# Optimization experiments

Measured on AMD Instinct MI355X. Metric: run time of the kernel, lower is better.

## Reference

```python
import jax, jax.numpy as jnp
import numpy as np

EPS = 1e-5


def setup_inputs() -> dict:
    key = jax.random.key(0)
    ks = jax.random.split(key, 12)
    B, S, M, D, H, dh = 8, 512, 512, 1024, 16, 64
    T = S + M
    w_scale = 0.03  # keep attention logits in a sane range (mimics nn.Linear init scale)
    return {
        "x": jax.random.normal(ks[0], (B, S, D), jnp.float32),
        "mem": jax.random.normal(ks[1], (B, M, D), jnp.float32),
        "R": jax.random.normal(ks[2], (T, D), jnp.float32),
        "u": jax.random.normal(ks[3], (1, H, 1, dh), jnp.float32) * 0.1,
        "t": jax.random.normal(ks[4], (1, H, 1, dh), jnp.float32) * 0.1,
        "Wq": jax.random.normal(ks[5], (H * dh, D), jnp.float32) * w_scale,
        "Wk": jax.random.normal(ks[6], (H * dh, D), jnp.float32) * w_scale,
        "Wv": jax.random.normal(ks[7], (H * dh, D), jnp.float32) * w_scale,
        "Wr": jax.random.normal(ks[8], (H * dh, D), jnp.float32) * w_scale,
        "Wo": jax.random.normal(ks[9], (D, H * dh), jnp.float32) * w_scale,
        "gamma": jnp.ones((D,), jnp.float32),
        "beta": jnp.zeros((D,), jnp.float32),
    }


def reference(x, mem, R, u, t, Wq, Wk, Wv, Wr, Wo, gamma, beta):
    B, S, D = x.shape
    H, dh = u.shape[1], u.shape[3]
    h = jnp.concatenate([mem, x], axis=1)          # [B, T, D]
    T = h.shape[1]
    M = T - S

    q = (x @ Wq.T).reshape(B, S, H, dh).transpose(0, 2, 1, 3)   # [B,H,S,dh]
    k = (h @ Wk.T).reshape(B, T, H, dh).transpose(0, 2, 1, 3)   # [B,H,T,dh]
    v = (h @ Wv.T).reshape(B, T, H, dh).transpose(0, 2, 1, 3)   # [B,H,T,dh]
    r = (R[-T:] @ Wr.T).reshape(1, T, H, dh).transpose(0, 2, 1, 3)  # [1,H,T,dh]

    ac = jnp.einsum("bhid,bhjd->bhij", q + u, k)                # [B,H,S,T]
    bd = jnp.einsum("bhid,hjd->bhij", q + t, r[0])              # [B,H,S,T]

    # circulant shift: shifted[..., i, j] = bd[..., i, (j - i + S - 1) % T]
    idx = (jnp.arange(T)[None, :] - jnp.arange(S)[:, None] + S - 1) % T  # [S,T]
    bd = jnp.take_along_axis(bd, idx[None, None], axis=3)

    # causal mask with memory offset: keep j <= i + M (tril(mem_len)), then
    # exact-zero entries (the masked ones) become -inf, matching the original.
    mask = jnp.arange(T)[None, :] <= (jnp.arange(S)[:, None] + M)        # [S,T]
    score = jnp.where(mask[None, None], (ac + bd) / jnp.sqrt(jnp.float32(dh)), 0.0)
    score = jnp.where(score == 0, -jnp.inf, score)
    p = jax.nn.softmax(score, axis=-1)                                   # [B,H,S,T]

    att = jnp.einsum("bhij,bhjd->bhid", p, v).transpose(0, 2, 1, 3).reshape(B, S, H * dh)
    out = att @ Wo.T                                                      # dropout is identity (p=0/eval)

    y = out + x
    mu = jnp.mean(y, axis=-1, keepdims=True)
    var = jnp.var(y, axis=-1, keepdims=True)
    return (y - mu) / jnp.sqrt(var + EPS) * gamma + beta
```

## Files before the change

### kernel.cpp

```cpp
#include <hip/hip_runtime.h>
#include <math.h>

#define BB 8
#define SS 512
#define MM 512
#define TT 1024
#define DD 1024
#define HH 16
#define DH 64

typedef __attribute__((ext_vector_type(8))) short bf16x8;
typedef __attribute__((ext_vector_type(4))) float f32x4;

#define SCL2E 0.1803368801111f
#define DTHR 11.5f

__device__ __forceinline__ ushort f2bf(float f) {
  union { float f; unsigned u; } x; x.f = f;
  unsigned r = x.u + 0x7fffu + ((x.u >> 16) & 1u);
  return (ushort)(r >> 16);
}
__device__ __forceinline__ float bf2f(ushort u) {
  return __builtin_bit_cast(float, ((unsigned)u) << 16);
}

__device__ __forceinline__ void stage16(void* lds, const void* g) {
  __builtin_amdgcn_global_load_lds((const __attribute__((address_space(1))) void*)g,
                                   (__attribute__((address_space(3))) void*)lds, 16, 0, 0);
}

template <int C>
__device__ __forceinline__ float dppf(float x) {
  return __builtin_bit_cast(float,
      __builtin_amdgcn_update_dpp(0, __builtin_bit_cast(int, x), C, 0xF, 0xF, true));
}
__device__ __forceinline__ float redmax16(float x) {
  x = fmaxf(x, dppf<0xB1>(x));
  x = fmaxf(x, dppf<0x4E>(x));
  x = fmaxf(x, dppf<0x141>(x));
  x = fmaxf(x, dppf<0x140>(x));
  return x;
}
__device__ __forceinline__ float redsum16(float x) {
  x += dppf<0xB1>(x);
  x += dppf<0x4E>(x);
  x += dppf<0x141>(x);
  x += dppf<0x140>(x);
  return x;
}
__device__ __forceinline__ float bperm_f(int byteaddr, float v) {
  return __builtin_bit_cast(float,
      __builtin_amdgcn_ds_bpermute(byteaddr, __builtin_bit_cast(int, v)));
}

__global__ __launch_bounds__(256) void cast_all(
    const float* __restrict__ mem, const float* __restrict__ x,
    const float* __restrict__ R, const float* __restrict__ Wq,
    const float* __restrict__ Wk, const float* __restrict__ Wv,
    const float* __restrict__ Wr, const float* __restrict__ Wo,
    ushort* __restrict__ hb, ushort* __restrict__ Rb, ushort* __restrict__ Wqb,
    ushort* __restrict__ Wkb, ushort* __restrict__ Wvb, ushort* __restrict__ Wrb,
    ushort* __restrict__ Wob) {
  const int M1 = 1 << 20;
  int i = (blockIdx.x * 256 + threadIdx.x) * 8;
  const float* src;
  ushort* dst;
  if (i < 4 * M1) {
    src = mem + i;
    dst = hb + (size_t)i + (size_t)(i >> 19) * 524288;
  } else if (i < 8 * M1) {
    int j = i - 4 * M1;
    src = x + j;
    dst = hb + (size_t)j + (size_t)(j >> 19) * 524288 + 524288;
  } else if (i < 9 * M1) {
    src = R + (i - 8 * M1);  dst = Rb + (i - 8 * M1);
  } else if (i < 10 * M1) {
    src = Wq + (i - 9 * M1); dst = Wqb + (i - 9 * M1);
  } else if (i < 11 * M1) {
    src = Wk + (i - 10 * M1); dst = Wkb + (i - 10 * M1);
  } else if (i < 12 * M1) {
    src = Wv + (i - 11 * M1); dst = Wvb + (i - 11 * M1);
  } else if (i < 13 * M1) {
    src = Wr + (i - 12 * M1); dst = Wrb + (i - 12 * M1);
  } else {
    src = Wo + (i - 13 * M1); dst = Wob + (i - 13 * M1);
  }
  float4 a = *(const float4*)(src);
  float4 c = *(const float4*)(src + 4);
  union { bf16x8 v; ushort u[8]; } pk;
  pk.u[0] = f2bf(a.x); pk.u[1] = f2bf(a.y); pk.u[2] = f2bf(a.z); pk.u[3] = f2bf(a.w);
  pk.u[4] = f2bf(c.x); pk.u[5] = f2bf(c.y); pk.u[6] = f2bf(c.z); pk.u[7] = f2bf(c.w);
  *(bf16x8*)(void*)dst = pk.v;
}

__global__ __launch_bounds__(256, 4) void gemm_qkvr(
    const ushort* __restrict__ hb, const ushort* __restrict__ Rbuf,
    const ushort* __restrict__ Wqb, const ushort* __restrict__ Wkb,
    const ushort* __restrict__ Wvb, const ushort* __restrict__ Wrb,
    ushort* __restrict__ qub,
    ushort* __restrict__ kbo, ushort* __restrict__ vtb, ushort* __restrict__ rbo,
    const float* __restrict__ uvec) {
  __shared__ ushort As0[4096], Bs0[4096], As1[4096], Bs1[4096];
  const int bid = (blockIdx.x & 7) * 168 + (blockIdx.x >> 3);
  const ushort* A;
  const ushort* W;
  ushort* C0 = nullptr;
  bool qadd = false, qslice = false, vmode = false;
  int mt, nx;
  if (bid < 256) {
    mt = bid >> 3; nx = bid & 7;
    A = hb; W = Wqb; C0 = qub; qadd = true; qslice = true;
  } else if (bid < 768) {
    int r = bid - 256; mt = r >> 3; nx = r & 7;
    A = hb; W = Wkb; C0 = kbo;
  } else if (bid < 1280) {
    int r = bid - 768; mt = r >> 3; nx = r & 7;
    A = hb; W = Wvb; C0 = vtb; vmode = true;
  } else {
    int r = bid - 1280; mt = r >> 3; nx = r & 7;
    A = Rbuf; W = Wrb; C0 = rbo;
  }
  const int m0 = mt * 128, n0 = nx * 128;

  const int t = threadIdx.x;
  const int w = t >> 6, l = t & 63;
  const int m16 = l & 15, kg = l >> 4;
  const int wr = w >> 1, wc = w & 1;

  const int c0 = t, c1 = t + 256;
  const int scol = (((t & 3) ^ ((t >> 3) & 3)) * 8);
  const ushort* asrc0;
  const ushort* asrc1;
  {
    int gm0 = m0 + (c0 >> 2), gm1 = m0 + (c1 >> 2);
    if (qslice) {
      asrc0 = A + ((size_t)((gm0 >> 9) * TT + MM + (gm0 & 511))) * DD + scol;
      asrc1 = A + ((size_t)((gm1 >> 9) * TT + MM + (gm1 & 511))) * DD + scol;
    } else {
      asrc0 = A + (size_t)gm0 * DD + scol;
      asrc1 = A + (size_t)gm1 * DD + scol;
    }
  }
  const ushort* bsrc0 = W + (size_t)(n0 + (c0 >> 2)) * DD + scol;
  const ushort* bsrc1 = W + (size_t)(n0 + (c1 >> 2)) * DD + scol;

  const int cbx = ((kg ^ ((m16 >> 1) & 3)) << 3);
  const int arow0 = (wr * 64 + m16) * 32 + cbx;
  const int brow0 = (wc * 64 + m16) * 32 + cbx;

  f32x4 acc[4][4];
#pragma unroll
  for (int mi = 0; mi < 4; ++mi)
#pragma unroll
    for (int ni = 0; ni < 4; ++ni) acc[mi][ni] = (f32x4){0.f, 0.f, 0.f, 0.f};

#define QKVR_STAGE(AS, BS, KOFF)                \
  do {                                          \
    stage16(AS + c0 * 8, asrc0 + (KOFF));       \
    stage16(AS + c1 * 8, asrc1 + (KOFF));       \
    stage16(BS + c0 * 8, bsrc0 + (KOFF));       \
    stage16(BS + c1 * 8, bsrc1 + (KOFF));       \
  } while (0)

#define QKVR_COMPUTE(AS, BS)                                                      \
  do {                                                                            \
    bf16x8 af[4], bfr[4];                                                         \
    _Pragma("unroll") for (int mi = 0; mi < 4; ++mi)                              \
        af[mi] = *(const bf16x8*)(const void*)&AS[arow0 + mi * 512];              \
    _Pragma("unroll") for (int ni = 0; ni < 4; ++ni)                              \
        bfr[ni] = *(const bf16x8*)(const void*)&BS[brow0 + ni * 512];             \
    _Pragma("unroll") for (int mi = 0; mi < 4; ++mi)                              \
        _Pragma("unroll") for (int ni = 0; ni < 4; ++ni)                          \
            acc[mi][ni] = __builtin_amdgcn_mfma_f32_16x16x32_bf16(                \
                af[mi], bfr[ni], acc[mi][ni], 0, 0, 0);                           \
  } while (0)

  QKVR_STAGE(As0, Bs0, 0);

#pragma unroll 1
  for (int kt = 0; kt < 32; kt += 2) {
    QKVR_STAGE(As1, Bs1, (kt + 1) << 5);
    asm volatile("s_waitcnt vmcnt(4)" ::: "memory");
    __builtin_amdgcn_s_barrier();
    QKVR_COMPUTE(As0, Bs0);
    __builtin_amdgcn_s_barrier();
    if (kt + 2 < 32) {
      QKVR_STAGE(As0, Bs0, (kt + 2) << 5);
      asm volatile("s_waitcnt vmcnt(4)" ::: "memory");
    } else {
      asm volatile("s_waitcnt vmcnt(0)" ::: "memory");
    }
    __builtin_amdgcn_s_barrier();
    QKVR_COMPUTE(As1, Bs1);
    __builtin_amdgcn_s_barrier();
  }
#undef QKVR_STAGE
#undef QKVR_COMPUTE

  const int rbase = m0 + wr * 64 + kg * 4;
  const int cbase = n0 + wc * 64 + m16;
  if (vmode) {
    const int bb = m0 >> 10;
    const int tt0 = (m0 & 1023) + wr * 64 + kg * 4;
#pragma unroll
    for (int mi = 0; mi < 4; ++mi)
#pragma unroll
      for (int ni = 0; ni < 4; ++ni) {
        ushort4 o;
        o.x = f2bf(acc[mi][ni][0]); o.y = f2bf(acc[mi][ni][1]);
        o.z = f2bf(acc[mi][ni][2]); o.w = f2bf(acc[mi][ni][3]);
        *(ushort4*)(C0 + ((size_t)(bb * 1024 + cbase + ni * 16) << 10) + tt0 + mi * 16) = o;
      }
  } else if (qadd) {
    float uv[4];
#pragma unroll
    for (int ni = 0; ni < 4; ++ni) uv[ni] = uvec[cbase + ni * 16];
#pragma unroll
    for (int mi = 0; mi < 4; ++mi)
#pragma unroll
      for (int ni = 0; ni < 4; ++ni)
#pragma unroll
        for (int rg = 0; rg < 4; ++rg)
          C0[(size_t)(rbase + mi * 16 + rg) * DD + cbase + ni * 16] = f2bf(acc[mi][ni][rg] + uv[ni]);
  } else {
#pragma unroll
    for (int mi = 0; mi < 4; ++mi)
#pragma unroll
      for (int ni = 0; ni < 4; ++ni)
#pragma unroll
        for (int rg = 0; rg < 4; ++rg)
          C0[(size_t)(rbase + mi * 16 + rg) * DD + cbase + ni * 16] = f2bf(acc[mi][ni][rg]);
  }
}

__global__ __launch_bounds__(256) void gemm_wo(const ushort* __restrict__ A,
                                               const ushort* __restrict__ W,
                                               ushort* __restrict__ Cb) {
  __shared__ ushort As[128 * 32];
  __shared__ ushort Bs[64 * 32];
  const int bid = (blockIdx.x & 7) * 64 + (blockIdx.x >> 3);
  const int mt = bid >> 4, nxt = bid & 15;
  const int m0 = mt * 128, n0 = nxt * 64;
  const int t = threadIdx.x;
  const int w = t >> 6, l = t & 63;
  const int m16 = l & 15, kg = l >> 4;
  const int wr = w >> 1, wc = w & 1;

  const int scol = (((t & 3) ^ ((t >> 3) & 3)) * 8);
  const ushort* asrc0 = A + (size_t)(m0 + (t >> 2)) * DD + scol;
  const ushort* asrc1 = A + (size_t)(m0 + 64 + (t >> 2)) * DD + scol;
  const ushort* bsrc0 = W + (size_t)(n0 + (t >> 2)) * DD + scol;
  ushort* adst0 = As + t * 8;
  ushort* adst1 = As + (t + 256) * 8;
  ushort* bdst0 = Bs + t * 8;

  const int cbx = ((kg ^ ((m16 >> 1) & 3)) << 3);

  f32x4 acc[4][2];
#pragma unroll
  for (int mi = 0; mi < 4; ++mi)
#pragma unroll
    for (int ni = 0; ni < 2; ++ni) acc[mi][ni] = (f32x4){0.f, 0.f, 0.f, 0.f};

  for (int k0 = 0; k0 < DD; k0 += 32) {
    stage16(adst0, asrc0 + k0);
    stage16(adst1, asrc1 + k0);
    stage16(bdst0, bsrc0 + k0);
    __syncthreads();
    bf16x8 af[4], bfr[2];
#pragma unroll
    for (int mi = 0; mi < 4; ++mi)
      af[mi] = *(const bf16x8*)(const void*)&As[(wr * 64 + mi * 16 + m16) * 32 + cbx];
#pragma unroll
    for (int ni = 0; ni < 2; ++ni)
      bfr[ni] = *(const bf16x8*)(const void*)&Bs[(wc * 32 + ni * 16 + m16) * 32 + cbx];
#pragma unroll
    for (int mi = 0; mi < 4; ++mi)
#pragma unroll
      for (int ni = 0; ni < 2; ++ni)
        acc[mi][ni] = __builtin_amdgcn_mfma_f32_16x16x32_bf16(af[mi], bfr[ni], acc[mi][ni], 0, 0, 0);
    __syncthreads();
  }

  const int rbase = m0 + wr * 64 + kg * 4;
  const int cbase = n0 + wc * 32 + m16;
#pragma unroll
  for (int mi = 0; mi < 4; ++mi)
#pragma unroll
    for (int ni = 0; ni < 2; ++ni)
#pragma unroll
      for (int rg = 0; rg < 4; ++rg)
        Cb[(size_t)(rbase + mi * 16 + rg) * DD + cbase + ni * 16] = f2bf(acc[mi][ni][rg]);
}

__global__ __launch_bounds__(256) void attn_mfma(const ushort* __restrict__ qu,
                                                 const ushort* __restrict__ kb,
                                                 const ushort* __restrict__ vt,
                                                 const ushort* __restrict__ rb,
                                                 const float* __restrict__ uvec,
                                                 const float* __restrict__ tvec,
                                                 ushort* __restrict__ att) {
  const int w = threadIdx.x >> 6;
  const int l = threadIdx.x & 63;
  const int m16 = l & 15;
  const int kg = l >> 4;
  const int bid = blockIdx.x;
  const int it = 7 - (bid >> 7);
  const int bh = bid & 127;
  const int b = bh >> 4, h = bh & 15;
  const int i0 = it * 64;

  __shared__ ushort Ks0[4096], Ks1[4096];
  __shared__ ushort Vs0[4096], Vs1[4096];
  __shared__ ushort Rl[16384];
  __shared__ ushort plds[4][16][72];

  bf16x8 aqu[2], aqt[2];
  {
    const ushort* qrow = qu + ((size_t)(b * SS + i0 + w * 16 + m16)) * DD + h * DH + kg * 8;
    aqu[0] = *(const bf16x8*)(const void*)(qrow);
    aqu[1] = *(const bf16x8*)(const void*)(qrow + 32);
#pragma unroll
    for (int ks = 0; ks < 2; ++ks) {
      ushort* a = (ushort*)&aqt[ks];
      const ushort* qa = (const ushort*)&aqu[ks];
#pragma unroll
      for (int e = 0; e < 8; ++e) {
        const int col = h * DH + kg * 8 + ks * 32 + e;
        a[e] = f2bf(bf2f(qa[e]) + (tvec[col] - uvec[col]));
      }
    }
  }

  int baddr[4];
  bool bsel[4];
#pragma unroll
  for (int rg = 0; rg < 4; ++rg) {
    const int rw = kg * 4 + rg;
    baddr[rg] = (kg * 16 + ((m16 + 15 - rw) & 15)) << 2;
    bsel[rg] = m16 > rw;
  }

  const int c0 = threadIdx.x, c1 = threadIdx.x + 256;
  const int r0 = c0 >> 3, sc0 = ((c0 & 7) * 8) ^ ((r0 & 7) << 3);
  const int r1 = c1 >> 3, sc1 = ((c1 & 7) * 8) ^ ((r1 & 7) << 3);
  const ushort* kp0 = kb + ((size_t)(b * TT) + r0) * DD + h * DH + sc0;
  const ushort* kp1 = kb + ((size_t)(b * TT) + r1) * DD + h * DH + sc1;
  const ushort* vp0 = vt + ((size_t)(b * 1024 + h * DH + r0)) * 1024 + sc0;
  const ushort* vp1 = vt + ((size_t)(b * 1024 + h * DH + r1)) * 1024 + sc1;

  const int cb0 = (kg * 8) ^ ((m16 & 7) << 3);
  const int cb1 = (kg * 8 + 32) ^ ((m16 & 7) << 3);
  int slot64[5];
#pragma unroll
  for (int f = 0; f < 5; ++f)
    slot64[f] = ((496 - i0 - w * 16 + m16 + f * 16) & 255) << 6;

  {
    const int base0 = 448 - i0;
#pragma unroll
    for (int kk = 0; kk < 4; ++kk) {
      int c = threadIdx.x + kk * 256;
      int ro = c >> 3, cc = c & 7;
      int p = base0 + ro;
      int slot = p & 255;
      stage16(Rl + slot * 64 + cc * 8,
              rb + (size_t)p * DD + h * DH + ((cc * 8) ^ ((ro & 7) << 3)));
    }
  }
  stage16(Ks0 + c0 * 8, kp0);
  stage16(Ks0 + c1 * 8, kp1);
  stage16(Vs0 + c0 * 8, vp0);
  stage16(Vs0 + c1 * 8, vp1);
  kp0 += (size_t)64 * DD; kp1 += (size_t)64 * DD;
  vp0 += 64; vp1 += 64;

  f32x4 O[4];
  float mrow[4], lrow[4];
#pragma unroll
  for (int nt = 0; nt < 4; ++nt) O[nt] = (f32x4){0.f, 0.f, 0.f, 0.f};
#pragma unroll
  for (int rg = 0; rg < 4; ++rg) { mrow[rg] = -1e30f; lrow[rg] = 0.f; }

  const int ntj = it + 9;

  auto stage_next = [&](ushort* KN, ushort* VN, int jt) {
    stage16(KN + c0 * 8, kp0);
    stage16(KN + c1 * 8, kp1);
    kp0 += (size_t)64 * DD; kp1 += (size_t)64 * DD;
    stage16(VN + c0 * 8, vp0);
    stage16(VN + c1 * 8, vp1);
    vp0 += 64; vp1 += 64;
    const int pstart = 576 + jt * 64 - i0;
#pragma unroll
    for (int kk = 0; kk < 2; ++kk) {
      int c = threadIdx.x + kk * 256;
      int ro = c >> 3, cc = c & 7;
      int p = pstart + ro;
      int pc = p < 1023 ? p : 1023;
      int slot = p & 255;
      stage16(Rl + slot * 64 + cc * 8,
              rb + (size_t)pc * DD + h * DH + ((cc * 8) ^ ((ro & 7) << 3)));
    }
  };

  auto compute_tile = [&](const ushort* kbase, const ushort* vbase, int jt) {
    const int j0 = jt * 64;
    f32x4 ac[4];
    __builtin_amdgcn_s_setprio(1);
#pragma unroll
    for (int nt = 0; nt < 4; ++nt) {
      ac[nt] = (f32x4){0.f, 0.f, 0.f, 0.f};
      const int row = nt * 16 + m16;
#pragma unroll
      for (int ks = 0; ks < 2; ++ks) {
        bf16x8 bk = *(const bf16x8*)(const void*)(kbase + row * 64 + (ks == 0 ? cb0 : cb1));
        ac[nt] = __builtin_amdgcn_mfma_f32_16x16x32_bf16(aqu[ks], bk, ac[nt], 0, 0, 0);
      }
    }
    f32x4 bd[5];
#pragma unroll
    for (int f = 0; f < 5; ++f) {
      f32x4 z = (f32x4){0.f, 0.f, 0.f, 0.f};
      bf16x8 b0 = *(const bf16x8*)(const void*)(Rl + slot64[f] + cb0);
      z = __builtin_amdgcn_mfma_f32_16x16x32_bf16(aqt[0], b0, z, 0, 0, 0);
      bf16x8 b1 = *(const bf16x8*)(const void*)(Rl + slot64[f] + cb1);
      bd[f] = __builtin_amdgcn_mfma_f32_16x16x32_bf16(aqt[1], b1, z, 0, 0, 0);
    }
    __builtin_amdgcn_s_setprio(0);
#pragma unroll
    for (int f = 0; f < 5; ++f) slot64[f] = (slot64[f] + 4096) & 16383;

    float sca[4][4];
#pragma unroll
    for (int rg = 0; rg < 4; ++rg) {
      float rr[5];
#pragma unroll
      for (int f = 0; f < 5; ++f) rr[f] = bperm_f(baddr[rg], bd[f][rg]);
#pragma unroll
      for (int nt = 0; nt < 4; ++nt) {
        float bdv = bsel[rg] ? rr[nt + 1] : rr[nt];
        sca[nt][rg] = (ac[nt][rg] + bdv) * SCL2E;
      }
    }
    if (jt == ntj - 1) {
#pragma unroll
      for (int rg = 0; rg < 4; ++rg) {
        const int jmax = i0 + w * 16 + kg * 4 + rg + MM;
#pragma unroll
        for (int nt = 0; nt < 4; ++nt)
          sca[nt][rg] = (j0 + nt * 16 + m16 <= jmax) ? sca[nt][rg] : -1e30f;
      }
    }

    float pmax[4];
#pragma unroll
    for (int rg = 0; rg < 4; ++rg) {
      float pm = fmaxf(fmaxf(sca[0][rg], sca[1][rg]), fmaxf(sca[2][rg], sca[3][rg]));
      pmax[rg] = redmax16(pm);
    }
    bool grow = false;
#pragma unroll
    for (int rg = 0; rg < 4; ++rg) grow = grow || (pmax[rg] > mrow[rg] + DTHR);
    if (__any(grow)) {
#pragma unroll
      for (int rg = 0; rg < 4; ++rg) {
        float mnew = fmaxf(mrow[rg], pmax[rg]);
        float scale = __builtin_amdgcn_exp2f(mrow[rg] - mnew);
        mrow[rg] = mnew;
        lrow[rg] *= scale;
#pragma unroll
        for (int nt = 0; nt < 4; ++nt) O[nt][rg] *= scale;
      }
    }

#pragma unroll
    for (int rg = 0; rg < 4; ++rg) {
      float ps = 0.f;
#pragma unroll
      for (int nt = 0; nt < 4; ++nt) {
        float p = __builtin_amdgcn_exp2f(sca[nt][rg] - mrow[rg]);
        ps += p;
        plds[w][kg * 4 + rg][nt * 16 + m16] = f2bf(p);
      }
      lrow[rg] += redsum16(ps);
    }

    __builtin_amdgcn_s_setprio(1);
#pragma unroll
    for (int ks = 0; ks < 2; ++ks) {
      bf16x8 pa = *(const bf16x8*)(const void*)&plds[w][m16][kg * 8 + ks * 32];
#pragma unroll
      for (int nt = 0; nt < 4; ++nt) {
        bf16x8 vf = *(const bf16x8*)(const void*)(vbase + (nt * 16 + m16) * 64 + (ks == 0 ? cb0 : cb1));
        O[nt] = __builtin_amdgcn_mfma_f32_16x16x32_bf16(pa, vf, O[nt], 0, 0, 0);
      }
    }
    __builtin_amdgcn_s_setprio(0);
  };

  int jt = 0;
  for (;;) {
    {
      if (jt + 1 < ntj) {
        stage_next(Ks1, Vs1, jt);
        asm volatile("s_waitcnt vmcnt(6)" ::: "memory");
      } else {
        asm volatile("s_waitcnt vmcnt(0)" ::: "memory");
      }
      __builtin_amdgcn_s_barrier();
      compute_tile(Ks0, Vs0, jt);
      if (jt + 1 == ntj) break;
      __builtin_amdgcn_s_barrier();
      ++jt;
    }
    {
      if (jt + 1 < ntj) {
        stage_next(Ks0, Vs0, jt);
        asm volatile("s_waitcnt vmcnt(6)" ::: "memory");
      } else {
        asm volatile("s_waitcnt vmcnt(0)" ::: "memory");
      }
      __builtin_amdgcn_s_barrier();
      compute_tile(Ks1, Vs1, jt);
      if (jt + 1 == ntj) break;
      __builtin_amdgcn_s_barrier();
      ++jt;
    }
  }

  float linv[4];
#pragma unroll
  for (int rg = 0; rg < 4; ++rg) linv[rg] = 1.f / lrow[rg];
#pragma unroll
  for (int nt = 0; nt < 4; ++nt) {
#pragma unroll
    for (int rg = 0; rg < 4; ++rg) {
      att[((size_t)(b * SS + i0 + w * 16 + kg * 4 + rg)) * DD + h * DH + nt * 16 + m16] =
          f2bf(O[nt][rg] * linv[rg]);
    }
  }
}

__global__ __launch_bounds__(256) void ln_kernel(const ushort* __restrict__ ypre,
                                                 const ushort* __restrict__ hb,
                                                 const float* __restrict__ gamma,
                                                 const float* __restrict__ beta,
                                                 float* __restrict__ out) {
  const int row = blockIdx.x;
  const int t = threadIdx.x;
  const int lane = t & 63, w = t >> 6;
  const ushort* yr = ypre + (size_t)row * DD;
  const ushort* xr = hb + ((size_t)((row >> 9) * TT + MM + (row & 511))) * DD;

  ushort4 yv = *(const ushort4*)(yr + t * 4);
  ushort4 xv = *(const ushort4*)(xr + t * 4);
  float v0 = bf2f(yv.x) + bf2f(xv.x), v1 = bf2f(yv.y) + bf2f(xv.y);
  float v2 = bf2f(yv.z) + bf2f(xv.z), v3 = bf2f(yv.w) + bf2f(xv.w);

  float s = v0 + v1 + v2 + v3;
  float ss = v0 * v0 + v1 * v1 + v2 * v2 + v3 * v3;
  __shared__ float rs[4], rss[4];
#pragma unroll
  for (int off = 32; off; off >>= 1) {
    s += __shfl_xor(s, off);
    ss += __shfl_xor(ss, off);
  }
  if (!lane) { rs[w] = s; rss[w] = ss; }
  __syncthreads();
  s = rs[0] + rs[1] + rs[2] + rs[3];
  ss = rss[0] + rss[1] + rss[2] + rss[3];
  const float mu = s * (1.f / DD);
  const float var = ss * (1.f / DD) - mu * mu;
  const float rstd = rsqrtf(var + 1e-5f);

  float4 g = *(const float4*)(gamma + t * 4);
  float4 be = *(const float4*)(beta + t * 4);
  float4 o;
  o.x = (v0 - mu) * rstd * g.x + be.x;
  o.y = (v1 - mu) * rstd * g.y + be.y;
  o.z = (v2 - mu) * rstd * g.z + be.z;
  o.w = (v3 - mu) * rstd * g.w + be.w;
  *(float4*)(out + (size_t)row * DD + t * 4) = o;
}

extern "C" void kernel_launch(void* const* d_in, const int* in_sizes, int n_in,
                              void* d_out, int out_size, void* d_ws, size_t ws_size,
                              hipStream_t stream) {
  const float* x = (const float*)d_in[0];
  const float* mem = (const float*)d_in[1];
  const float* R = (const float*)d_in[2];
  const float* u = (const float*)d_in[3];
  const float* tv = (const float*)d_in[4];
  const float* Wq = (const float*)d_in[5];
  const float* Wk = (const float*)d_in[6];
  const float* Wv = (const float*)d_in[7];
  const float* Wr = (const float*)d_in[8];
  const float* Wo = (const float*)d_in[9];
  const float* gamma = (const float*)d_in[10];
  const float* beta = (const float*)d_in[11];
  float* out = (float*)d_out;

  ushort* hb = (ushort*)d_ws;
  ushort* Rb = hb + (8u << 20);
  ushort* Wqb = Rb + (1u << 20);
  ushort* Wkb = Wqb + (1u << 20);
  ushort* Wvb = Wkb + (1u << 20);
  ushort* Wrb = Wvb + (1u << 20);
  ushort* Wob = Wrb + (1u << 20);
  ushort* qu_b = Wob + (1u << 20);
  ushort* kb = qu_b + (4u << 20);
  ushort* vt = kb + (8u << 20);
  ushort* rb = vt + (8u << 20);
  ushort* att = qu_b;
  ushort* ypre = kb;

  dim3 blk(256);

  cast_all<<<dim3(7168), blk, 0, stream>>>(mem, x, R, Wq, Wk, Wv, Wr, Wo,
                                           hb, Rb, Wqb, Wkb, Wvb, Wrb, Wob);

  gemm_qkvr<<<dim3(1344), blk, 0, stream>>>(hb, Rb, Wqb, Wkb, Wvb, Wrb,
                                            qu_b, kb, vt, rb, u);

  attn_mfma<<<dim3(BB * HH * 8), blk, 0, stream>>>(qu_b, kb, vt, rb, u, tv, att);

  gemm_wo<<<dim3(512), blk, 0, stream>>>(att, Wob, ypre);

  ln_kernel<<<dim3(BB * SS), blk, 0, stream>>>(ypre, hb, gamma, beta, out);
}
```

Baseline: 158.3 us.

## Fuse K and V projections into one GEMM block sharing the A tile

Blocks that computed the K and V projections now compute both in one pass: each block stages the h tile once and multiplies it against both Wk and Wv tiles, keeping two accumulator sets. This halves A-tile global loads and LDS staging for the K/V part and cuts the grid from 1344 to 832 blocks. In exchange, register use doubles for those blocks (launch bounds lowered to 2 blocks per SM), LDS per block grows to 48KB, and the work per block becomes uneven between K/V blocks and Q/R blocks.

```diff
diff --git a/kernel.cpp b/kernel.cpp
--- a/kernel.cpp
+++ b/kernel.cpp
@@ -93,32 +93,31 @@
   *(bf16x8*)(void*)dst = pk.v;
 }
 
-__global__ __launch_bounds__(256, 4) void gemm_qkvr(
+__global__ __launch_bounds__(256, 2) void gemm_qkvr(
     const ushort* __restrict__ hb, const ushort* __restrict__ Rbuf,
     const ushort* __restrict__ Wqb, const ushort* __restrict__ Wkb,
     const ushort* __restrict__ Wvb, const ushort* __restrict__ Wrb,
     ushort* __restrict__ qub,
     ushort* __restrict__ kbo, ushort* __restrict__ vtb, ushort* __restrict__ rbo,
     const float* __restrict__ uvec) {
-  __shared__ ushort As0[4096], Bs0[4096], As1[4096], Bs1[4096];
-  const int bid = (blockIdx.x & 7) * 168 + (blockIdx.x >> 3);
+  __shared__ ushort As0[4096], As1[4096], Bk0[4096], Bk1[4096], Bv0[4096], Bv1[4096];
+  const int bid = (blockIdx.x & 7) * 104 + (blockIdx.x >> 3);
   const ushort* A;
-  const ushort* W;
+  const ushort* Wk_;
+  const ushort* Wv_ = nullptr;
   ushort* C0 = nullptr;
-  bool qadd = false, qslice = false, vmode = false;
+  ushort* C1 = nullptr;
+  bool qadd = false, qslice = false, kvmode = false;
   int mt, nx;
   if (bid < 256) {
     mt = bid >> 3; nx = bid & 7;
-    A = hb; W = Wqb; C0 = qub; qadd = true; qslice = true;
+    A = hb; Wk_ = Wqb; C0 = qub; qadd = true; qslice = true;
   } else if (bid < 768) {
-    int r = bid - 256; mt = r >> 3; nx = r & 7;
-    A = hb; W = Wkb; C0 = kbo;
-  } else if (bid < 1280) {
-    int r = bid - 768; mt = r >> 3; nx = r & 7;
-    A = hb; W = Wvb; C0 = vtb; vmode = true;
+    int r2 = bid - 256; mt = r2 >> 3; nx = r2 & 7;
+    A = hb; Wk_ = Wkb; Wv_ = Wvb; C0 = kbo; C1 = vtb; kvmode = true;
   } else {
-    int r = bid - 1280; mt = r >> 3; nx = r & 7;
-    A = Rbuf; W = Wrb; C0 = rbo;
+    int r2 = bid - 768; mt = r2 >> 3; nx = r2 & 7;
+    A = Rbuf; Wk_ = Wrb; C0 = rbo;
   }
   const int m0 = mt * 128, n0 = nx * 128;
 
@@ -141,28 +140,40 @@
       asrc1 = A + (size_t)gm1 * DD + scol;
     }
   }
-  const ushort* bsrc0 = W + (size_t)(n0 + (c0 >> 2)) * DD + scol;
-  const ushort* bsrc1 = W + (size_t)(n0 + (c1 >> 2)) * DD + scol;
+  const ushort* bksrc0 = Wk_ + (size_t)(n0 + (c0 >> 2)) * DD + scol;
+  const ushort* bksrc1 = Wk_ + (size_t)(n0 + (c1 >> 2)) * DD + scol;
+  const ushort* bvsrc0 = kvmode ? Wv_ + (size_t)(n0 + (c0 >> 2)) * DD + scol : nullptr;
+  const ushort* bvsrc1 = kvmode ? Wv_ + (size_t)(n0 + (c1 >> 2)) * DD + scol : nullptr;
 
   const int cbx = ((kg ^ ((m16 >> 1) & 3)) << 3);
   const int arow0 = (wr * 64 + m16) * 32 + cbx;
   const int brow0 = (wc * 64 + m16) * 32 + cbx;
 
-  f32x4 acc[4][4];
+  f32x4 acck[4][4], accv[4][4];
 #pragma unroll
   for (int mi = 0; mi < 4; ++mi)
 #pragma unroll
-    for (int ni = 0; ni < 4; ++ni) acc[mi][ni] = (f32x4){0.f, 0.f, 0.f, 0.f};
-
-#define QKVR_STAGE(AS, BS, KOFF)                \
+    for (int ni = 0; ni < 4; ++ni) {
+      acck[mi][ni] = (f32x4){0.f, 0.f, 0.f, 0.f};
+      accv[mi][ni] = (f32x4){0.f, 0.f, 0.f, 0.f};
+    }
+
+#define ST4(AS, BS, KOFF)                       \
   do {                                          \
     stage16(AS + c0 * 8, asrc0 + (KOFF));       \
     stage16(AS + c1 * 8, asrc1 + (KOFF));       \
-    stage16(BS + c0 * 8, bsrc0 + (KOFF));       \
-    stage16(BS + c1 * 8, bsrc1 + (KOFF));       \
+    stage16(BS + c0 * 8, bksrc0 + (KOFF));      \
+    stage16(BS + c1 * 8, bksrc1 + (KOFF));      \
   } while (0)
 
-#define QKVR_COMPUTE(AS, BS)                                                      \
+#define ST6(AS, BS, BV, KOFF)                   \
+  do {                                          \
+    ST4(AS, BS, KOFF);                          \
+    stage16(BV + c0 * 8, bvsrc0 + (KOFF));      \
+    stage16(BV + c1 * 8, bvsrc1 + (KOFF));      \
+  } while (0)
+
+#define CMP1(AS, BS)                                                              \
   do {                                                                            \
     bf16x8 af[4], bfr[4];                                                         \
     _Pragma("unroll") for (int mi = 0; mi < 4; ++mi)                              \
@@ -171,35 +182,83 @@
         bfr[ni] = *(const bf16x8*)(const void*)&BS[brow0 + ni * 512];             \
     _Pragma("unroll") for (int mi = 0; mi < 4; ++mi)                              \
         _Pragma("unroll") for (int ni = 0; ni < 4; ++ni)                          \
-            acc[mi][ni] = __builtin_amdgcn_mfma_f32_16x16x32_bf16(                \
-                af[mi], bfr[ni], acc[mi][ni], 0, 0, 0);                           \
+            acck[mi][ni] = __builtin_amdgcn_mfma_f32_16x16x32_bf16(               \
+                af[mi], bfr[ni], acck[mi][ni], 0, 0, 0);                          \
   } while (0)
 
-  QKVR_STAGE(As0, Bs0, 0);
-
+#define CMP2(AS, BS, BV)                                                          \
+  do {                                                                            \
+    bf16x8 af[4], bfk[4], bfv[4];                                                 \
+    _Pragma("unroll") for (int mi = 0; mi < 4; ++mi)                              \
+        af[mi] = *(const bf16x8*)(const void*)&AS[arow0 + mi * 512];              \
+    _Pragma("unroll") for (int ni = 0; ni < 4; ++ni)                              \
+        bfk[ni] = *(const bf16x8*)(const void*)&BS[brow0 + ni * 512];             \
+    _Pragma("unroll") for (int ni = 0; ni < 4; ++ni)                              \
+        bfv[ni] = *(const bf16x8*)(const void*)&BV[brow0 + ni * 512];             \
+    _Pragma("unroll") for (int mi = 0; mi < 4; ++mi)                              \
+        _Pragma("unroll") for (int ni = 0; ni < 4; ++ni)                          \
+            acck[mi][ni] = __builtin_amdgcn_mfma_f32_16x16x32_bf16(               \
+                af[mi], bfk[ni], acck[mi][ni], 0, 0, 0);                          \
+    _Pragma("unroll") for (int mi = 0; mi < 4; ++mi)                              \
+        _Pragma("unroll") for (int ni = 0; ni < 4; ++ni)                          \
+            accv[mi][ni] = __builtin_amdgcn_mfma_f32_16x16x32_bf16(               \
+                af[mi], bfv[ni], accv[mi][ni], 0, 0, 0);                          \
+  } while (0)
+
+  if (kvmode) {
+    ST6(As0, Bk0, Bv0, 0);
 #pragma unroll 1
-  for (int kt = 0; kt < 32; kt += 2) {
-    QKVR_STAGE(As1, Bs1, (kt + 1) << 5);
-    asm volatile("s_waitcnt vmcnt(4)" ::: "memory");
-    __builtin_amdgcn_s_barrier();
-    QKVR_COMPUTE(As0, Bs0);
-    __builtin_amdgcn_s_barrier();
-    if (kt + 2 < 32) {
-      QKVR_STAGE(As0, Bs0, (kt + 2) << 5);
+    for (int kt = 0; kt < 32; kt += 2) {
+      ST6(As1, Bk1, Bv1, (kt + 1) << 5);
+      asm volatile("s_waitcnt vmcnt(6)" ::: "memory");
+      __builtin_amdgcn_s_barrier();
+      CMP2(As0, Bk0, Bv0);
+      __builtin_amdgcn_s_barrier();
+      if (kt + 2 < 32) {
+        ST6(As0, Bk0, Bv0, (kt + 2) << 5);
+        asm volatile("s_waitcnt vmcnt(6)" ::: "memory");
+      } else {
+        asm volatile("s_waitcnt vmcnt(0)" ::: "memory");
+      }
+      __builtin_amdgcn_s_barrier();
+      CMP2(As1, Bk1, Bv1);
+      __builtin_amdgcn_s_barrier();
+    }
+  } else {
+    ST4(As0, Bk0, 0);
+#pragma unroll 1
+    for (int kt = 0; kt < 32; kt += 2) {
+      ST4(As1, Bk1, (kt + 1) << 5);
       asm volatile("s_waitcnt vmcnt(4)" ::: "memory");
-    } else {
-      asm volatile("s_waitcnt vmcnt(0)" ::: "memory");
-    }
-    __builtin_amdgcn_s_barrier();
-    QKVR_COMPUTE(As1, Bs1);
-    __builtin_amdgcn_s_barrier();
-  }
-#undef QKVR_STAGE
-#undef QKVR_COMPUTE
+      __builtin_amdgcn_s_barrier();
+      CMP1(As0, Bk0);
+      __builtin_amdgcn_s_barrier();
+      if (kt + 2 < 32) {
+        ST4(As0, Bk0, (kt + 2) << 5);
+        asm volatile("s_waitcnt vmcnt(4)" ::: "memory");
+      } else {
+        asm volatile("s_waitcnt vmcnt(0)" ::: "memory");
+      }
+      __builtin_amdgcn_s_barrier();
+      CMP1(As1, Bk1);
+      __builtin_amdgcn_s_barrier();
+    }
+  }
+#undef ST4
+#undef ST6
+#undef CMP1
+#undef CMP2
 
   const int rbase = m0 + wr * 64 + kg * 4;
   const int cbase = n0 + wc * 64 + m16;
-  if (vmode) {
+  if (kvmode) {
+#pragma unroll
+    for (int mi = 0; mi < 4; ++mi)
+#pragma unroll
+      for (int ni = 0; ni < 4; ++ni)
+#pragma unroll
+        for (int rg = 0; rg < 4; ++rg)
+          C0[(size_t)(rbase + mi * 16 + rg) * DD + cbase + ni * 16] = f2bf(acck[mi][ni][rg]);
     const int bb = m0 >> 10;
     const int tt0 = (m0 & 1023) + wr * 64 + kg * 4;
 #pragma unroll
@@ -207,9 +266,9 @@
 #pragma unroll
       for (int ni = 0; ni < 4; ++ni) {
         ushort4 o;
-        o.x = f2bf(acc[mi][ni][0]); o.y = f2bf(acc[mi][ni][1]);
-        o.z = f2bf(acc[mi][ni][2]); o.w = f2bf(acc[mi][ni][3]);
-        *(ushort4*)(C0 + ((size_t)(bb * 1024 + cbase + ni * 16) << 10) + tt0 + mi * 16) = o;
+        o.x = f2bf(accv[mi][ni][0]); o.y = f2bf(accv[mi][ni][1]);
+        o.z = f2bf(accv[mi][ni][2]); o.w = f2bf(accv[mi][ni][3]);
+        *(ushort4*)(C1 + ((size_t)(bb * 1024 + cbase + ni * 16) << 10) + tt0 + mi * 16) = o;
       }
   } else if (qadd) {
     float uv[4];
@@ -221,7 +280,7 @@
       for (int ni = 0; ni < 4; ++ni)
 #pragma unroll
         for (int rg = 0; rg < 4; ++rg)
-          C0[(size_t)(rbase + mi * 16 + rg) * DD + cbase + ni * 16] = f2bf(acc[mi][ni][rg] + uv[ni]);
+          C0[(size_t)(rbase + mi * 16 + rg) * DD + cbase + ni * 16] = f2bf(acck[mi][ni][rg] + uv[ni]);
   } else {
 #pragma unroll
     for (int mi = 0; mi < 4; ++mi)
@@ -229,7 +288,7 @@
       for (int ni = 0; ni < 4; ++ni)
 #pragma unroll
         for (int rg = 0; rg < 4; ++rg)
-          C0[(size_t)(rbase + mi * 16 + rg) * DD + cbase + ni * 16] = f2bf(acc[mi][ni][rg]);
+          C0[(size_t)(rbase + mi * 16 + rg) * DD + cbase + ni * 16] = f2bf(acck[mi][ni][rg]);
   }
 }
 
@@ -620,8 +679,8 @@
   cast_all<<<dim3(7168), blk, 0, stream>>>(mem, x, R, Wq, Wk, Wv, Wr, Wo,
                                            hb, Rb, Wqb, Wkb, Wvb, Wrb, Wob);
 
-  gemm_qkvr<<<dim3(1344), blk, 0, stream>>>(hb, Rb, Wqb, Wkb, Wvb, Wrb,
-                                            qu_b, kb, vt, rb, u);
+  gemm_qkvr<<<dim3(832), blk, 0, stream>>>(hb, Rb, Wqb, Wkb, Wvb, Wrb,
+                                           qu_b, kb, vt, rb, u);
 
   attn_mfma<<<dim3(BB * HH * 8), blk, 0, stream>>>(qu_b, kb, vt, rb, u, tv, att);
 
```

Result: slower. 168.3 us (+6.4%).

## Double-buffer LDS staging in Wo projection GEMM with async wait counts

Applied to the files above, without the earlier changes.

The output-projection GEMM now keeps two LDS buffers for the A and W tiles. It issues the global-to-LDS loads for the next K slice before computing on the current one, using explicit vmcnt waits and raw barriers. This is meant to hide global load latency behind the MFMA work instead of stalling at every K step. The cost is double the LDS footprint and reliance on stage16 being an async direct-to-LDS load whose counter semantics match vmcnt(3).

```diff
diff --git a/kernel.cpp b/kernel.cpp
--- a/kernel.cpp
+++ b/kernel.cpp
@@ -236,8 +236,7 @@
 __global__ __launch_bounds__(256) void gemm_wo(const ushort* __restrict__ A,
                                                const ushort* __restrict__ W,
                                                ushort* __restrict__ Cb) {
-  __shared__ ushort As[128 * 32];
-  __shared__ ushort Bs[64 * 32];
+  __shared__ ushort As0[4096], As1[4096], Bs0[2048], Bs1[2048];
   const int bid = (blockIdx.x & 7) * 64 + (blockIdx.x >> 3);
   const int mt = bid >> 4, nxt = bid & 15;
   const int m0 = mt * 128, n0 = nxt * 64;
@@ -250,11 +249,10 @@
   const ushort* asrc0 = A + (size_t)(m0 + (t >> 2)) * DD + scol;
   const ushort* asrc1 = A + (size_t)(m0 + 64 + (t >> 2)) * DD + scol;
   const ushort* bsrc0 = W + (size_t)(n0 + (t >> 2)) * DD + scol;
-  ushort* adst0 = As + t * 8;
-  ushort* adst1 = As + (t + 256) * 8;
-  ushort* bdst0 = Bs + t * 8;
 
   const int cbx = ((kg ^ ((m16 >> 1) & 3)) << 3);
+  const int arow0 = (wr * 64 + m16) * 32 + cbx;
+  const int brow0 = (wc * 32 + m16) * 32 + cbx;
 
   f32x4 acc[4][2];
 #pragma unroll
@@ -262,25 +260,47 @@
 #pragma unroll
     for (int ni = 0; ni < 2; ++ni) acc[mi][ni] = (f32x4){0.f, 0.f, 0.f, 0.f};
 
-  for (int k0 = 0; k0 < DD; k0 += 32) {
-    stage16(adst0, asrc0 + k0);
-    stage16(adst1, asrc1 + k0);
-    stage16(bdst0, bsrc0 + k0);
-    __syncthreads();
-    bf16x8 af[4], bfr[2];
-#pragma unroll
-    for (int mi = 0; mi < 4; ++mi)
-      af[mi] = *(const bf16x8*)(const void*)&As[(wr * 64 + mi * 16 + m16) * 32 + cbx];
-#pragma unroll
-    for (int ni = 0; ni < 2; ++ni)
-      bfr[ni] = *(const bf16x8*)(const void*)&Bs[(wc * 32 + ni * 16 + m16) * 32 + cbx];
-#pragma unroll
-    for (int mi = 0; mi < 4; ++mi)
-#pragma unroll
-      for (int ni = 0; ni < 2; ++ni)
-        acc[mi][ni] = __builtin_amdgcn_mfma_f32_16x16x32_bf16(af[mi], bfr[ni], acc[mi][ni], 0, 0, 0);
-    __syncthreads();
-  }
+#define WO_STAGE(AS, BS, KOFF)                    \
+  do {                                            \
+    stage16(AS + t * 8, asrc0 + (KOFF));          \
+    stage16(AS + (t + 256) * 8, asrc1 + (KOFF));  \
+    stage16(BS + t * 8, bsrc0 + (KOFF));          \
+  } while (0)
+
+#define WO_COMPUTE(AS, BS)                                                        \
+  do {                                                                            \
+    bf16x8 af[4], bfr[2];                                                         \
+    _Pragma("unroll") for (int mi = 0; mi < 4; ++mi)                              \
+        af[mi] = *(const bf16x8*)(const void*)&AS[arow0 + mi * 512];              \
+    _Pragma("unroll") for (int ni = 0; ni < 2; ++ni)                              \
+        bfr[ni] = *(const bf16x8*)(const void*)&BS[brow0 + ni * 512];             \
+    _Pragma("unroll") for (int mi = 0; mi < 4; ++mi)                              \
+        _Pragma("unroll") for (int ni = 0; ni < 2; ++ni)                          \
+            acc[mi][ni] = __builtin_amdgcn_mfma_f32_16x16x32_bf16(                \
+                af[mi], bfr[ni], acc[mi][ni], 0, 0, 0);                           \
+  } while (0)
+
+  WO_STAGE(As0, Bs0, 0);
+
+#pragma unroll 1
+  for (int kt = 0; kt < 32; kt += 2) {
+    WO_STAGE(As1, Bs1, (kt + 1) << 5);
+    asm volatile("s_waitcnt vmcnt(3)" ::: "memory");
+    __builtin_amdgcn_s_barrier();
+    WO_COMPUTE(As0, Bs0);
+    __builtin_amdgcn_s_barrier();
+    if (kt + 2 < 32) {
+      WO_STAGE(As0, Bs0, (kt + 2) << 5);
+      asm volatile("s_waitcnt vmcnt(3)" ::: "memory");
+    } else {
+      asm volatile("s_waitcnt vmcnt(0)" ::: "memory");
+    }
+    __builtin_amdgcn_s_barrier();
+    WO_COMPUTE(As1, Bs1);
+    __builtin_amdgcn_s_barrier();
+  }
+#undef WO_STAGE
+#undef WO_COMPUTE
 
   const int rbase = m0 + wr * 64 + kg * 4;
   const int cbase = n0 + wc * 32 + m16;
```

After: 157.6 us. About the same (-0.4%).
